# Performance work log

Measured on AMD Instinct MI355X. Metric: run time of the kernel, lower is better.

## Reference

```python
import jax, jax.numpy as jnp
import numpy as np

K = 16
TAU = 1.0
EPSILON = float(np.finfo(np.float32).tiny)


def setup_inputs() -> dict:
    key = jax.random.key(0)
    k1, k2 = jax.random.split(key)
    scores = jax.random.normal(k1, (4096, 8192), dtype=jnp.float32)
    # Gumbel(0,1) noise, sampled outside forward for determinism
    g = jax.random.gumbel(k2, (4096, 8192), dtype=jnp.float32)
    return {"scores": scores, "g": g}


def reference(scores, g):
    # scores, g: [B, N]
    s0 = scores + g
    zeros = jnp.zeros_like(s0)

    def step(carry, _):
        s, khot, onehot = carry
        khot_mask = jnp.maximum(1.0 - onehot, EPSILON)
        s = s + jnp.log(khot_mask)
        onehot = jax.nn.softmax(s / TAU, axis=1)
        khot = khot + onehot
        return (s, khot, onehot), None

    (_, khot, _), _ = jax.lax.scan(step, (s0, zeros, zeros), None, length=K)
    return khot  # hard=False -> soft k-hot relaxation, rows sum to ~k
```

## Files before the change

kernel.cpp:

```cpp
#include <hip/hip_runtime.h>


constexpr int N_COLS  = 8192;
constexpr int THREADS = 512;
constexpr int PER     = N_COLS / THREADS;
constexpr int ROWS_PB = 2;
constexpr int NWAVES  = THREADS / 64;
constexpr int KITER   = 16;

template<int PAT>
__device__ __forceinline__ float swz_add(float v) {
    int s = __builtin_amdgcn_ds_swizzle(__float_as_int(v), PAT);
    return v + __int_as_float(s);
}

__device__ __forceinline__ float tree16(const float* v) {
    return (((v[0] + v[1]) + (v[2] + v[3])) + ((v[4] + v[5]) + (v[6] + v[7])))
         + (((v[8] + v[9]) + (v[10] + v[11])) + ((v[12] + v[13]) + (v[14] + v[15])));
}

__global__ __launch_bounds__(THREADS, 4)
void subset_op_kernel(const float* __restrict__ scores,
                      const float* __restrict__ gnoise,
                      float* __restrict__ out)
{
    const int t    = threadIdx.x;
    const int wave = t >> 6;
    const int lane = t & 63;
    const size_t base = (size_t)blockIdx.x * (size_t)(ROWS_PB * N_COLS);
    constexpr int ROW4 = N_COLS / 4;

    const float4* s4 = (const float4*)(scores + base);
    const float4* g4 = (const float4*)(gnoise + base);
    float4*       o4 = (float4*)(out + base);

    float e0[PER], e1[PER], kh0[PER], kh1[PER];

    #pragma unroll
    for (int c = 0; c < PER / 4; ++c) {
        float4 a  = s4[c * THREADS + t];
        float4 b  = g4[c * THREADS + t];
        e0[c*4 + 0] = __expf(a.x + b.x);
        e0[c*4 + 1] = __expf(a.y + b.y);
        e0[c*4 + 2] = __expf(a.z + b.z);
        e0[c*4 + 3] = __expf(a.w + b.w);
        float4 a2 = s4[ROW4 + c * THREADS + t];
        float4 b2 = g4[ROW4 + c * THREADS + t];
        e1[c*4 + 0] = __expf(a2.x + b2.x);
        e1[c*4 + 1] = __expf(a2.y + b2.y);
        e1[c*4 + 2] = __expf(a2.z + b2.z);
        e1[c*4 + 3] = __expf(a2.w + b2.w);
    }
    #pragma unroll
    for (int j = 0; j < PER; ++j) { kh0[j] = 0.0f; kh1[j] = 0.0f; }

    float z0 = tree16(e0);
    float z1 = tree16(e1);

    __shared__ float2 red[2][2 * NWAVES];

    #pragma unroll 2
    for (int it = 0; it < KITER; ++it) {
        float r0 = z0, r1 = z1;
        r0 = swz_add<0x041F>(r0);  r1 = swz_add<0x041F>(r1);
        r0 = swz_add<0x081F>(r0);  r1 = swz_add<0x081F>(r1);
        r0 = swz_add<0x101F>(r0);  r1 = swz_add<0x101F>(r1);
        r0 = swz_add<0x201F>(r0);  r1 = swz_add<0x201F>(r1);
        r0 = swz_add<0x401F>(r0);  r1 = swz_add<0x401F>(r1);
        if ((lane & 31) == 0)
            red[it & 1][wave * 2 + (lane >> 5)] = make_float2(r0, r1);
        __syncthreads();

        float Z0, Z1;
        {
            const float4* rp = (const float4*)(&red[it & 1][0]);
            float4 v0 = rp[0], v1 = rp[1], v2 = rp[2], v3 = rp[3];
            float4 v4 = rp[4], v5 = rp[5], v6 = rp[6], v7 = rp[7];
            Z0 = (((v0.x + v0.z) + (v1.x + v1.z)) + ((v2.x + v2.z) + (v3.x + v3.z)))
               + (((v4.x + v4.z) + (v5.x + v5.z)) + ((v6.x + v6.z) + (v7.x + v7.z)));
            Z1 = (((v0.y + v0.w) + (v1.y + v1.w)) + ((v2.y + v2.w) + (v3.y + v3.w)))
               + (((v4.y + v4.w) + (v5.y + v5.w)) + ((v6.y + v6.w) + (v7.y + v7.w)));
        }
        const float inv0 = __builtin_amdgcn_rcpf(Z0);
        const float inv1 = __builtin_amdgcn_rcpf(Z1);

        float za[4] = {0.f, 0.f, 0.f, 0.f};
        float zb[4] = {0.f, 0.f, 0.f, 0.f};
        #pragma unroll
        for (int j = 0; j < PER; ++j) {
            float oh0 = e0[j] * inv0;
            kh0[j] += oh0;
            e0[j] = __builtin_fmaf(-oh0, e0[j], e0[j]);
            za[j & 3] += e0[j];
            float oh1 = e1[j] * inv1;
            kh1[j] += oh1;
            e1[j] = __builtin_fmaf(-oh1, e1[j], e1[j]);
            zb[j & 3] += e1[j];
        }
        z0 = (za[0] + za[1]) + (za[2] + za[3]);
        z1 = (zb[0] + zb[1]) + (zb[2] + zb[3]);
    }

    #pragma unroll
    for (int c = 0; c < PER / 4; ++c) {
        float4 v, w;
        v.x = kh0[c*4 + 0]; v.y = kh0[c*4 + 1]; v.z = kh0[c*4 + 2]; v.w = kh0[c*4 + 3];
        w.x = kh1[c*4 + 0]; w.y = kh1[c*4 + 1]; w.z = kh1[c*4 + 2]; w.w = kh1[c*4 + 3];
        o4[c * THREADS + t]        = v;
        o4[ROW4 + c * THREADS + t] = w;
    }
}

extern "C" void kernel_launch(void* const* d_in, const int* in_sizes, int n_in,
                              void* d_out, int out_size, void* d_ws, size_t ws_size,
                              hipStream_t stream)
{
    const float* scores = (const float*)d_in[0];
    const float* gnoise = (const float*)d_in[1];
    float* out = (float*)d_out;
    const int rows = in_sizes[0] / N_COLS;

    subset_op_kernel<<<rows / ROWS_PB, THREADS, 0, stream>>>(scores, gnoise, out);
}
```

Before: 329.8 us.

## Replay k-hot accumulation from saved inverses to cut register pressure

```diff
diff --git a/kernel.cpp b/kernel.cpp
--- a/kernel.cpp
+++ b/kernel.cpp
@@ -14,12 +14,16 @@
     return v + __int_as_float(s);
 }
 
+__device__ __forceinline__ float rfl(float v) {
+    return __int_as_float(__builtin_amdgcn_readfirstlane(__float_as_int(v)));
+}
+
 __device__ __forceinline__ float tree16(const float* v) {
     return (((v[0] + v[1]) + (v[2] + v[3])) + ((v[4] + v[5]) + (v[6] + v[7])))
          + (((v[8] + v[9]) + (v[10] + v[11])) + ((v[12] + v[13]) + (v[14] + v[15])));
 }
 
-__global__ __launch_bounds__(THREADS, 4)
+__global__ __launch_bounds__(THREADS, 8)
 void subset_op_kernel(const float* __restrict__ scores,
                       const float* __restrict__ gnoise,
                       float* __restrict__ out)
@@ -34,7 +38,7 @@
     const float4* g4 = (const float4*)(gnoise + base);
     float4*       o4 = (float4*)(out + base);
 
-    float e0[PER], e1[PER], kh0[PER], kh1[PER];
+    float e0[PER], e1[PER];
 
     #pragma unroll
     for (int c = 0; c < PER / 4; ++c) {
@@ -51,15 +55,15 @@
         e1[c*4 + 2] = __expf(a2.z + b2.z);
         e1[c*4 + 3] = __expf(a2.w + b2.w);
     }
-    #pragma unroll
-    for (int j = 0; j < PER; ++j) { kh0[j] = 0.0f; kh1[j] = 0.0f; }
 
     float z0 = tree16(e0);
     float z1 = tree16(e1);
 
-    __shared__ float2 red[2][2 * NWAVES];
+    __shared__ float2 red[2][NWAVES];
 
-    #pragma unroll 2
+    float iv0[KITER], iv1[KITER];
+
+    #pragma unroll
     for (int it = 0; it < KITER; ++it) {
         float r0 = z0, r1 = z1;
         r0 = swz_add<0x041F>(r0);  r1 = swz_add<0x041F>(r1);
@@ -67,45 +71,72 @@
         r0 = swz_add<0x101F>(r0);  r1 = swz_add<0x101F>(r1);
         r0 = swz_add<0x201F>(r0);  r1 = swz_add<0x201F>(r1);
         r0 = swz_add<0x401F>(r0);  r1 = swz_add<0x401F>(r1);
-        if ((lane & 31) == 0)
-            red[it & 1][wave * 2 + (lane >> 5)] = make_float2(r0, r1);
+        r0 += __shfl_xor(r0, 32, 64);
+        r1 += __shfl_xor(r1, 32, 64);
+        if (lane == 0) red[it & 1][wave] = make_float2(r0, r1);
         __syncthreads();
 
         float Z0, Z1;
         {
             const float4* rp = (const float4*)(&red[it & 1][0]);
             float4 v0 = rp[0], v1 = rp[1], v2 = rp[2], v3 = rp[3];
-            float4 v4 = rp[4], v5 = rp[5], v6 = rp[6], v7 = rp[7];
-            Z0 = (((v0.x + v0.z) + (v1.x + v1.z)) + ((v2.x + v2.z) + (v3.x + v3.z)))
-               + (((v4.x + v4.z) + (v5.x + v5.z)) + ((v6.x + v6.z) + (v7.x + v7.z)));
-            Z1 = (((v0.y + v0.w) + (v1.y + v1.w)) + ((v2.y + v2.w) + (v3.y + v3.w)))
-               + (((v4.y + v4.w) + (v5.y + v5.w)) + ((v6.y + v6.w) + (v7.y + v7.w)));
+            Z0 = ((v0.x + v0.z) + (v1.x + v1.z)) + ((v2.x + v2.z) + (v3.x + v3.z));
+            Z1 = ((v0.y + v0.w) + (v1.y + v1.w)) + ((v2.y + v2.w) + (v3.y + v3.w));
         }
-        const float inv0 = __builtin_amdgcn_rcpf(Z0);
-        const float inv1 = __builtin_amdgcn_rcpf(Z1);
+        const float i0 = rfl(__builtin_amdgcn_rcpf(Z0));
+        const float i1 = rfl(__builtin_amdgcn_rcpf(Z1));
+        iv0[it] = i0;
+        iv1[it] = i1;
 
-        float za[4] = {0.f, 0.f, 0.f, 0.f};
-        float zb[4] = {0.f, 0.f, 0.f, 0.f};
-        #pragma unroll
-        for (int j = 0; j < PER; ++j) {
-            float oh0 = e0[j] * inv0;
-            kh0[j] += oh0;
-            e0[j] = __builtin_fmaf(-oh0, e0[j], e0[j]);
-            za[j & 3] += e0[j];
-            float oh1 = e1[j] * inv1;
-            kh1[j] += oh1;
-            e1[j] = __builtin_fmaf(-oh1, e1[j], e1[j]);
-            zb[j & 3] += e1[j];
+        if (it < KITER - 1) {
+            float za[4] = {0.f, 0.f, 0.f, 0.f};
+            float zb[4] = {0.f, 0.f, 0.f, 0.f};
+            #pragma unroll
+            for (int j = 0; j < PER; ++j) {
+                float oh0 = e0[j] * i0;
+                e0[j] = __builtin_fmaf(-oh0, e0[j], e0[j]);
+                za[j & 3] += e0[j];
+                float oh1 = e1[j] * i1;
+                e1[j] = __builtin_fmaf(-oh1, e1[j], e1[j]);
+                zb[j & 3] += e1[j];
+            }
+            z0 = (za[0] + za[1]) + (za[2] + za[3]);
+            z1 = (zb[0] + zb[1]) + (zb[2] + zb[3]);
         }
-        z0 = (za[0] + za[1]) + (za[2] + za[3]);
-        z1 = (zb[0] + zb[1]) + (zb[2] + zb[3]);
     }
 
     #pragma unroll
     for (int c = 0; c < PER / 4; ++c) {
+        float4 a  = s4[c * THREADS + t];
+        float4 b  = g4[c * THREADS + t];
+        float4 a2 = s4[ROW4 + c * THREADS + t];
+        float4 b2 = g4[ROW4 + c * THREADS + t];
+        float p[8], kh[8];
+        p[0] = __expf(a.x + b.x);   p[1] = __expf(a.y + b.y);
+        p[2] = __expf(a.z + b.z);   p[3] = __expf(a.w + b.w);
+        p[4] = __expf(a2.x + b2.x); p[5] = __expf(a2.y + b2.y);
+        p[6] = __expf(a2.z + b2.z); p[7] = __expf(a2.w + b2.w);
+        #pragma unroll
+        for (int q = 0; q < 8; ++q) kh[q] = 0.0f;
+
+        #pragma unroll
+        for (int it = 0; it < KITER; ++it) {
+            const float u0 = iv0[it];
+            const float u1 = iv1[it];
+            #pragma unroll
+            for (int q = 0; q < 4; ++q) {
+                float oh0 = p[q] * u0;
+                kh[q] += oh0;
+                p[q] = __builtin_fmaf(-oh0, p[q], p[q]);
+                float oh1 = p[4 + q] * u1;
+                kh[4 + q] += oh1;
+                p[4 + q] = __builtin_fmaf(-oh1, p[4 + q], p[4 + q]);
+            }
+        }
+
         float4 v, w;
-        v.x = kh0[c*4 + 0]; v.y = kh0[c*4 + 1]; v.z = kh0[c*4 + 2]; v.w = kh0[c*4 + 3];
-        w.x = kh1[c*4 + 0]; w.y = kh1[c*4 + 1]; w.z = kh1[c*4 + 2]; w.w = kh1[c*4 + 3];
+        v.x = kh[0]; v.y = kh[1]; v.z = kh[2]; v.w = kh[3];
+        w.x = kh[4]; w.y = kh[5]; w.z = kh[6]; w.w = kh[7];
         o4[c * THREADS + t]        = v;
         o4[ROW4 + c * THREADS + t] = w;
     }
```

Measured after the change: 339.1 us. 1.03x slower.

## Process one row per block with full unroll and higher occupancy

Applied to the files above, without the earlier changes.

```diff
diff --git a/kernel.cpp b/kernel.cpp
--- a/kernel.cpp
+++ b/kernel.cpp
@@ -4,7 +4,6 @@
 constexpr int N_COLS  = 8192;
 constexpr int THREADS = 512;
 constexpr int PER     = N_COLS / THREADS;
-constexpr int ROWS_PB = 2;
 constexpr int NWAVES  = THREADS / 64;
 constexpr int KITER   = 16;
 
@@ -14,12 +13,16 @@
     return v + __int_as_float(s);
 }
 
+__device__ __forceinline__ float rfl(float v) {
+    return __int_as_float(__builtin_amdgcn_readfirstlane(__float_as_int(v)));
+}
+
 __device__ __forceinline__ float tree16(const float* v) {
     return (((v[0] + v[1]) + (v[2] + v[3])) + ((v[4] + v[5]) + (v[6] + v[7])))
          + (((v[8] + v[9]) + (v[10] + v[11])) + ((v[12] + v[13]) + (v[14] + v[15])));
 }
 
-__global__ __launch_bounds__(THREADS, 4)
+__global__ __launch_bounds__(THREADS, 8)
 void subset_op_kernel(const float* __restrict__ scores,
                       const float* __restrict__ gnoise,
                       float* __restrict__ out)
@@ -27,87 +30,73 @@
     const int t    = threadIdx.x;
     const int wave = t >> 6;
     const int lane = t & 63;
-    const size_t base = (size_t)blockIdx.x * (size_t)(ROWS_PB * N_COLS);
-    constexpr int ROW4 = N_COLS / 4;
+    const size_t base = (size_t)blockIdx.x * (size_t)N_COLS;
 
     const float4* s4 = (const float4*)(scores + base);
     const float4* g4 = (const float4*)(gnoise + base);
     float4*       o4 = (float4*)(out + base);
 
-    float e0[PER], e1[PER], kh0[PER], kh1[PER];
+    float e[PER], kh[PER];
 
     #pragma unroll
     for (int c = 0; c < PER / 4; ++c) {
-        float4 a  = s4[c * THREADS + t];
-        float4 b  = g4[c * THREADS + t];
-        e0[c*4 + 0] = __expf(a.x + b.x);
-        e0[c*4 + 1] = __expf(a.y + b.y);
-        e0[c*4 + 2] = __expf(a.z + b.z);
-        e0[c*4 + 3] = __expf(a.w + b.w);
-        float4 a2 = s4[ROW4 + c * THREADS + t];
-        float4 b2 = g4[ROW4 + c * THREADS + t];
-        e1[c*4 + 0] = __expf(a2.x + b2.x);
-        e1[c*4 + 1] = __expf(a2.y + b2.y);
-        e1[c*4 + 2] = __expf(a2.z + b2.z);
-        e1[c*4 + 3] = __expf(a2.w + b2.w);
+        float4 a = s4[c * THREADS + t];
+        float4 b = g4[c * THREADS + t];
+        e[c*4 + 0] = __expf(a.x + b.x);
+        e[c*4 + 1] = __expf(a.y + b.y);
+        e[c*4 + 2] = __expf(a.z + b.z);
+        e[c*4 + 3] = __expf(a.w + b.w);
     }
     #pragma unroll
-    for (int j = 0; j < PER; ++j) { kh0[j] = 0.0f; kh1[j] = 0.0f; }
+    for (int j = 0; j < PER; ++j) kh[j] = 0.0f;
 
-    float z0 = tree16(e0);
-    float z1 = tree16(e1);
+    float z = tree16(e);
 
-    __shared__ float2 red[2][2 * NWAVES];
+    __shared__ float red[2][NWAVES];
 
-    #pragma unroll 2
+    #pragma unroll
     for (int it = 0; it < KITER; ++it) {
-        float r0 = z0, r1 = z1;
-        r0 = swz_add<0x041F>(r0);  r1 = swz_add<0x041F>(r1);
-        r0 = swz_add<0x081F>(r0);  r1 = swz_add<0x081F>(r1);
-        r0 = swz_add<0x101F>(r0);  r1 = swz_add<0x101F>(r1);
-        r0 = swz_add<0x201F>(r0);  r1 = swz_add<0x201F>(r1);
-        r0 = swz_add<0x401F>(r0);  r1 = swz_add<0x401F>(r1);
-        if ((lane & 31) == 0)
-            red[it & 1][wave * 2 + (lane >> 5)] = make_float2(r0, r1);
+        float r = z;
+        r = swz_add<0x041F>(r);
+        r = swz_add<0x081F>(r);
+        r = swz_add<0x101F>(r);
+        r = swz_add<0x201F>(r);
+        r = swz_add<0x401F>(r);
+        r += __shfl_xor(r, 32, 64);
+        if (lane == 0) red[it & 1][wave] = r;
         __syncthreads();
 
-        float Z0, Z1;
+        float Z;
         {
             const float4* rp = (const float4*)(&red[it & 1][0]);
-            float4 v0 = rp[0], v1 = rp[1], v2 = rp[2], v3 = rp[3];
-            float4 v4 = rp[4], v5 = rp[5], v6 = rp[6], v7 = rp[7];
-            Z0 = (((v0.x + v0.z) + (v1.x + v1.z)) + ((v2.x + v2.z) + (v3.x + v3.z)))
-               + (((v4.x + v4.z) + (v5.x + v5.z)) + ((v6.x + v6.z) + (v7.x + v7.z)));
-            Z1 = (((v0.y + v0.w) + (v1.y + v1.w)) + ((v2.y + v2.w) + (v3.y + v3.w)))
-               + (((v4.y + v4.w) + (v5.y + v5.w)) + ((v6.y + v6.w) + (v7.y + v7.w)));
+            float4 v0 = rp[0], v1 = rp[1];
+            Z = ((v0.x + v0.y) + (v0.z + v0.w)) + ((v1.x + v1.y) + (v1.z + v1.w));
         }
-        const float inv0 = __builtin_amdgcn_rcpf(Z0);
-        const float inv1 = __builtin_amdgcn_rcpf(Z1);
+        const float inv = rfl(__builtin_amdgcn_rcpf(Z));
 
-        float za[4] = {0.f, 0.f, 0.f, 0.f};
-        float zb[4] = {0.f, 0.f, 0.f, 0.f};
-        #pragma unroll
-        for (int j = 0; j < PER; ++j) {
-            float oh0 = e0[j] * inv0;
-            kh0[j] += oh0;
-            e0[j] = __builtin_fmaf(-oh0, e0[j], e0[j]);
-            za[j & 3] += e0[j];
-            float oh1 = e1[j] * inv1;
-            kh1[j] += oh1;
-            e1[j] = __builtin_fmaf(-oh1, e1[j], e1[j]);
-            zb[j & 3] += e1[j];
+        if (it < KITER - 1) {
+            float za[4] = {0.f, 0.f, 0.f, 0.f};
+            #pragma unroll
+            for (int j = 0; j < PER; ++j) {
+                float oh = e[j] * inv;
+                kh[j] += oh;
+                e[j] = __builtin_fmaf(-oh, e[j], e[j]);
+                za[j & 3] += e[j];
+            }
+            z = (za[0] + za[1]) + (za[2] + za[3]);
+        } else {
+            #pragma unroll
+            for (int j = 0; j < PER; ++j)
+                kh[j] = __builtin_fmaf(e[j], inv, kh[j]);
         }
-        z0 = (za[0] + za[1]) + (za[2] + za[3]);
-        z1 = (zb[0] + zb[1]) + (zb[2] + zb[3]);
     }
 
     #pragma unroll
     for (int c = 0; c < PER / 4; ++c) {
-        float4 v, w;
-        v.x = kh0[c*4 + 0]; v.y = kh0[c*4 + 1]; v.z = kh0[c*4 + 2]; v.w = kh0[c*4 + 3];
-        w.x = kh1[c*4 + 0]; w.y = kh1[c*4 + 1]; w.z = kh1[c*4 + 2]; w.w = kh1[c*4 + 3];
-        o4[c * THREADS + t]        = v;
-        o4[ROW4 + c * THREADS + t] = w;
+        float4 v;
+        v.x = kh[c*4 + 0]; v.y = kh[c*4 + 1];
+        v.z = kh[c*4 + 2]; v.w = kh[c*4 + 3];
+        o4[c * THREADS + t] = v;
     }
 }
 
@@ -120,5 +109,5 @@
     float* out = (float*)d_out;
     const int rows = in_sizes[0] / N_COLS;
 
-    subset_op_kernel<<<rows / ROWS_PB, THREADS, 0, stream>>>(scores, gnoise, out);
+    subset_op_kernel<<<rows, THREADS, 0, stream>>>(scores, gnoise, out);
 }
```

Result: slower. 952.7 us (+188.9%).
